# Kernel tuning notes

Measured on AMD Instinct MI355X. Metric: run time of the kernel, lower is better.

## Reference

```python
import jax, jax.numpy as jnp
import numpy as np
from jax import lax

B, S, E, DF, H, L, V, T = 32, 512, 512, 2048, 8, 2, 30000, 12
START, STOP = 10, 11
NEG = -10000.0


def setup_inputs() -> dict:
    key = jax.random.key(0)
    ks = jax.random.split(key, 12)
    g = lambda i, shape, sc=0.02: jax.random.normal(ks[i], shape, jnp.float32) * sc
    trans = jax.random.normal(ks[9], (T, T), jnp.float32)
    trans = trans.at[START, :].set(NEG).at[:, STOP].set(NEG)
    return {
        "sentence": jax.random.randint(ks[0], (B, S), 0, V),
        "seq_len": jax.random.randint(ks[1], (B,), 1, S + 1),
        "tags": jax.random.randint(ks[2], (B, S), 0, 10),
        "emb": g(3, (V, E), 1.0),
        "attn_in_w": g(4, (L, 3 * E, E)), "attn_in_b": jnp.zeros((L, 3 * E)),
        "attn_out_w": g(5, (L, E, E)), "attn_out_b": jnp.zeros((L, E)),
        "ln1_g": jnp.ones((L, E)), "ln1_b": jnp.zeros((L, E)),
        "ln2_g": jnp.ones((L, E)), "ln2_b": jnp.zeros((L, E)),
        "ff1_w": g(6, (L, DF, E)), "ff1_b": jnp.zeros((L, DF)),
        "ff2_w": g(7, (L, E, DF)), "ff2_b": jnp.zeros((L, E)),
        "tag_w": g(8, (T, E)), "tag_b": jnp.zeros((T,)),
        "transitions": trans,
    }


def _ln(x, g, b):
    m = x.mean(-1, keepdims=True)
    v = ((x - m) ** 2).mean(-1, keepdims=True)
    return (x - m) / jnp.sqrt(v + 1e-5) * g + b


def _mha(x, w_in, b_in, w_out, b_out):
    b_, s_, e_ = x.shape
    d = e_ // H
    qkv = x @ w_in.T + b_in
    q, k, v = jnp.split(qkv, 3, axis=-1)
    split = lambda t: t.reshape(b_, s_, H, d).transpose(0, 2, 1, 3)
    q, k, v = split(q), split(k), split(v)
    att = jax.nn.softmax(jnp.einsum('bhqd,bhkd->bhqk', q, k) / np.sqrt(d).astype(np.float32), axis=-1)
    o = jnp.einsum('bhqk,bhkd->bhqd', att, v).transpose(0, 2, 1, 3).reshape(b_, s_, e_)
    return o @ w_out.T + b_out


def _forward_impl(sentence, seq_len, tags, emb, attn_in_w, attn_in_b, attn_out_w,
                  attn_out_b, ln1_g, ln1_b, ln2_g, ln2_b, ff1_w, ff1_b, ff2_w,
                  ff2_b, tag_w, tag_b, transitions):
    # Transformer encoder features (dropout in eval mode -> identity)
    x = emb[sentence]  # (B,S,E)
    for l in range(L):
        x = _ln(x + _mha(x, attn_in_w[l], attn_in_b[l], attn_out_w[l], attn_out_b[l]), ln1_g[l], ln1_b[l])
        h = jax.nn.relu(x @ ff1_w[l].T + ff1_b[l]) @ ff2_w[l].T + ff2_b[l]
        x = _ln(x + h, ln2_g[l], ln2_b[l])
    feats = x @ tag_w.T + tag_b  # (B,S,T)

    # CRF forward algorithm (log-semiring scan, masked by seq_len)
    alpha0 = jnp.full((B, T), NEG, feats.dtype).at[:, START].set(0.0)

    def step(alpha, xs):
        emit_t, t = xs  # emit_t: (B,T)
        new = emit_t + jax.nn.logsumexp(alpha[:, None, :] + transitions[None, :, :], axis=-1)
        return jnp.where((t < seq_len)[:, None], new, alpha), None

    alpha, _ = lax.scan(step, alpha0, (feats.transpose(1, 0, 2), jnp.arange(S)))
    fwd_score = jax.nn.logsumexp(alpha + transitions[STOP][None, :], axis=-1)  # (B,)

    # gold score (vectorized _score_sentence)
    tags_ext = jnp.concatenate([jnp.full((B, 1), START, tags.dtype), tags], axis=1)  # (B,S+1)
    mask = jnp.arange(S)[None, :] < seq_len[:, None]  # (B,S)
    trans_sc = jnp.where(mask, transitions[tags_ext[:, 1:], tags_ext[:, :-1]], 0.0).sum(-1)
    emit_sc = jnp.where(mask, jnp.take_along_axis(feats, tags[:, :, None], axis=2)[..., 0], 0.0).sum(-1)
    last_tag = jnp.take_along_axis(tags_ext, seq_len[:, None], axis=1)[:, 0]
    gold = trans_sc + emit_sc + transitions[STOP, last_tag]

    return jnp.mean(fwd_score - gold)


def reference(sentence, seq_len, tags, emb, attn_in_w, attn_in_b, attn_out_w,
              attn_out_b, ln1_g, ln1_b, ln2_g, ln2_b, ff1_w, ff1_b, ff2_w,
              ff2_b, tag_w, tag_b, transitions):
    return _forward_impl(sentence, seq_len, tags, emb, attn_in_w, attn_in_b,
                         attn_out_w, attn_out_b, ln1_g, ln1_b, ln2_g, ln2_b,
                         ff1_w, ff1_b, ff2_w, ff2_b, tag_w, tag_b, transitions)
```

## Files before the change

### kernel.cpp

```cpp
#include <hip/hip_runtime.h>
#include <hip/hip_bf16.h>

#define BB 32
#define SSZ 512
#define EE 512
#define DFF 2048
#define HH 8
#define LL 2
#define TT 12
#define START_TAG 10
#define STOP_TAG 11
#define CB 8
#define CM (CB * SSZ)
#define NCHUNK (BB / CB)
#define NBH (CB * HH)
#define NBH_ALL (BB * HH)
#define NCHK 8

typedef __hip_bfloat16 bf16;
typedef __attribute__((ext_vector_type(8))) short short8;
typedef __attribute__((ext_vector_type(4))) float f32x4;

__device__ __forceinline__ float b2f(bf16 x) { return __bfloat162float(x); }
__device__ __forceinline__ float ldw(const void* p, size_t i, bool isbf) {
  return isbf ? __bfloat162float(((const bf16*)p)[i]) : ((const float*)p)[i];
}

__device__ __forceinline__ void gl_lds16(const bf16* g, bf16* l) {
  __builtin_amdgcn_global_load_lds(
      (const __attribute__((address_space(1))) void*)g,
      (__attribute__((address_space(3))) void*)l, 16, 0, 0);
}

__global__ void k_detect(const void* trans, int* dflag) {
  if (threadIdx.x == 0) {
    const unsigned short* u = (const unsigned short*)trans;
    dflag[0] = (u[START_TAG * TT] == 0xC61C && u[START_TAG * TT + 1] == 0xC61C) ? 1 : 0;
  }
}

__global__ void k_cvt(const void* src, bf16* dst, long n, const int* dflag) {
  bool isbf = dflag[0] != 0;
  for (long i = (long)blockIdx.x * 256 + threadIdx.x; i < n; i += (long)gridDim.x * 256)
    dst[i] = __float2bfloat16(ldw(src, i, isbf));
}

__global__ void k_embed(const int* sent, const void* emb, bf16* xb, const int* dflag) {
  bool isbf = dflag[0] != 0;
  int tok = blockIdx.x;
  int v = sent[tok];
  bf16* xo = xb + (size_t)tok * EE;
  for (int i = threadIdx.x; i < EE; i += 256)
    xo[i] = __float2bfloat16(ldw(emb, (size_t)v * EE + i, isbf));
}

__global__ __launch_bounds__(256) void k_mgemm(
    const bf16* __restrict__ A, const bf16* __restrict__ W,
    const void* __restrict__ bias, size_t boff, bf16* __restrict__ Cb,
    int M, int N, int K, int relu, const int* dflag) {
  bool isbf = dflag[0] != 0;
  __shared__ __align__(16) bf16 Sh[2 * 128 * 64];
  bf16* As = Sh;
  bf16* Bs = Sh + 128 * 64;
  const int tid = threadIdx.x;
  const int lane = tid & 63;
  const int wave = tid >> 6;
  const int wm = wave >> 1, wn = wave & 1;
  const int m0 = blockIdx.x * 128, n0 = blockIdx.y * 128;
  const int lrow = lane & 15, lk = lane >> 4;
  const int rl = lane >> 3, sl = lane & 7;

  f32x4 acc[4][4];
#pragma unroll
  for (int i = 0; i < 4; ++i)
#pragma unroll
    for (int j = 0; j < 4; ++j) acc[i][j] = (f32x4){0.f, 0.f, 0.f, 0.f};

  for (int kt = 0; kt < K; kt += 64) {
#pragma unroll
    for (int i = 0; i < 4; ++i) {
      int r = wave * 32 + i * 8 + rl;
      int gs = sl ^ (r & 7);
      gl_lds16(A + (size_t)(m0 + r) * K + kt + gs * 8, As + wave * 2048 + i * 512);
      gl_lds16(W + (size_t)(n0 + r) * K + kt + gs * 8, Bs + wave * 2048 + i * 512);
    }
    __syncthreads();
#pragma unroll
    for (int kb = 0; kb < 64; kb += 32) {
      short8 af[4], bfr[4];
#pragma unroll
      for (int mf = 0; mf < 4; ++mf) {
        int r = wm * 64 + mf * 16 + lrow;
        int ps = ((kb >> 3) + lk) ^ (r & 7);
        af[mf] = *(const short8*)&As[r * 64 + ps * 8];
      }
#pragma unroll
      for (int nf = 0; nf < 4; ++nf) {
        int r = wn * 64 + nf * 16 + lrow;
        int ps = ((kb >> 3) + lk) ^ (r & 7);
        bfr[nf] = *(const short8*)&Bs[r * 64 + ps * 8];
      }
#pragma unroll
      for (int mf = 0; mf < 4; ++mf)
#pragma unroll
        for (int nf = 0; nf < 4; ++nf)
          acc[mf][nf] = __builtin_amdgcn_mfma_f32_16x16x32_bf16(
              af[mf], bfr[nf], acc[mf][nf], 0, 0, 0);
    }
    __syncthreads();
  }
#pragma unroll
  for (int nf = 0; nf < 4; ++nf) {
    int nl = wn * 64 + nf * 16 + lrow;
    float bia = ldw(bias, boff + n0 + nl, isbf);
#pragma unroll
    for (int mf = 0; mf < 4; ++mf) {
#pragma unroll
      for (int r = 0; r < 4; ++r) {
        int ml = wm * 64 + mf * 16 + lk * 4 + r;
        float v = acc[mf][nf][r] + bia;
        if (relu) v = fmaxf(v, 0.f);
        Sh[ml * 128 + nl] = __float2bfloat16(v);
      }
    }
  }
  __syncthreads();
#pragma unroll
  for (int p = 0; p < 8; ++p) {
    int row = p * 16 + (tid >> 4);
    int off = (tid & 15) * 8;
    *(uint4*)(Cb + (size_t)(m0 + row) * N + n0 + off) = *(const uint4*)&Sh[row * 128 + off];
  }
}

__global__ void k_vt(const bf16* __restrict__ qkvb, bf16* __restrict__ vt) {
  int bh = blockIdx.y;
  int bl = bh >> 3, h = bh & 7;
  int k0 = blockIdx.x * 64;
  __shared__ bf16 t[64][72];
  int tid = threadIdx.x;
  int r = tid >> 2, cg = (tid & 3) * 16;
  const bf16* src = qkvb + ((size_t)(bl * SSZ + k0 + r)) * 1536 + 1024 + h * 64 + cg;
  *(uint4*)&t[r][cg] = *(const uint4*)src;
  *(uint4*)&t[r][cg + 8] = *(const uint4*)(src + 8);
  __syncthreads();
  int d = tid >> 2, kg = (tid & 3) * 16;
  bf16 tmp[16];
#pragma unroll
  for (int j = 0; j < 16; ++j) tmp[j] = t[kg + j][d];
  bf16* dst = vt + ((size_t)bh * 64 + d) * 512 + k0 + kg;
  *(uint4*)dst = *(uint4*)&tmp[0];
  *(uint4*)(dst + 8) = *(uint4*)&tmp[8];
}

#define LDK 68
#define LDP 72
__global__ __launch_bounds__(256) void k_flash(const bf16* __restrict__ qkv,
                                               const bf16* __restrict__ vt,
                                               bf16* __restrict__ ctx) {
  const int bh = blockIdx.x;
  const int bl = bh >> 3, h = bh & 7;
  const int m0 = blockIdx.y * 128;
  const int tid = threadIdx.x;
  const int lane = tid & 63;
  const int w = tid >> 6;
  const int lrow = lane & 15, lk = lane >> 4;

  __shared__ bf16 Ks[64 * LDK];
  __shared__ bf16 Vs[64 * LDK];
  __shared__ bf16 Ps[4][32 * LDP];

  short8 qf[2][2];
  {
    const bf16* Qb = qkv + (size_t)(bl * SSZ + m0 + w * 32) * 1536 + h * 64;
#pragma unroll
    for (int mf = 0; mf < 2; ++mf)
#pragma unroll
      for (int kb = 0; kb < 2; ++kb)
        qf[mf][kb] = *(const short8*)(Qb + (size_t)(mf * 16 + lrow) * 1536 + kb * 32 + lk * 8);
  }

  f32x4 acc_o[2][4];
  float lsum[2][4];
#pragma unroll
  for (int mf = 0; mf < 2; ++mf) {
#pragma unroll
    for (int nf = 0; nf < 4; ++nf) acc_o[mf][nf] = (f32x4){0.f, 0.f, 0.f, 0.f};
#pragma unroll
    for (int r = 0; r < 4; ++r) lsum[mf][r] = 0.f;
  }

  for (int kt = 0; kt < 8; ++kt) {
#pragma unroll
    for (int i = 0; i < 2; ++i) {
      int cc = tid + i * 256;
      int row = cc >> 3, seg = cc & 7;
      *(uint4*)&Ks[row * LDK + seg * 8] = *(const uint4*)(
          qkv + (size_t)(bl * SSZ + kt * 64 + row) * 1536 + 512 + h * 64 + seg * 8);
      *(uint4*)&Vs[row * LDK + seg * 8] = *(const uint4*)(
          vt + ((size_t)bh * 64 + row) * SSZ + kt * 64 + seg * 8);
    }
    __syncthreads();
    f32x4 s[2][4];
#pragma unroll
    for (int mf = 0; mf < 2; ++mf)
#pragma unroll
      for (int nf = 0; nf < 4; ++nf) s[mf][nf] = (f32x4){0.f, 0.f, 0.f, 0.f};
#pragma unroll
    for (int kb = 0; kb < 2; ++kb) {
      short8 bk[4];
#pragma unroll
      for (int nf = 0; nf < 4; ++nf)
        bk[nf] = *(const short8*)&Ks[(nf * 16 + lrow) * LDK + kb * 32 + lk * 8];
#pragma unroll
      for (int mf = 0; mf < 2; ++mf)
#pragma unroll
        for (int nf = 0; nf < 4; ++nf)
          s[mf][nf] = __builtin_amdgcn_mfma_f32_16x16x32_bf16(qf[mf][kb], bk[nf],
                                                              s[mf][nf], 0, 0, 0);
    }
#pragma unroll
    for (int mf = 0; mf < 2; ++mf)
#pragma unroll
      for (int r = 0; r < 4; ++r) {
        float p0 = __expf(0.125f * s[mf][0][r]);
        float p1 = __expf(0.125f * s[mf][1][r]);
        float p2 = __expf(0.125f * s[mf][2][r]);
        float p3 = __expf(0.125f * s[mf][3][r]);
        s[mf][0][r] = p0; s[mf][1][r] = p1; s[mf][2][r] = p2; s[mf][3][r] = p3;
        lsum[mf][r] += (p0 + p1) + (p2 + p3);
      }
#pragma unroll
    for (int mf = 0; mf < 2; ++mf)
#pragma unroll
      for (int nf = 0; nf < 4; ++nf)
#pragma unroll
        for (int r = 0; r < 4; ++r)
          Ps[w][(mf * 16 + lk * 4 + r) * LDP + nf * 16 + lrow] =
              __float2bfloat16(s[mf][nf][r]);
#pragma unroll
    for (int kb = 0; kb < 2; ++kb) {
      short8 ap[2], bv[4];
#pragma unroll
      for (int mf = 0; mf < 2; ++mf)
        ap[mf] = *(const short8*)&Ps[w][(mf * 16 + lrow) * LDP + kb * 32 + lk * 8];
#pragma unroll
      for (int nf = 0; nf < 4; ++nf)
        bv[nf] = *(const short8*)&Vs[(nf * 16 + lrow) * LDK + kb * 32 + lk * 8];
#pragma unroll
      for (int mf = 0; mf < 2; ++mf)
#pragma unroll
        for (int nf = 0; nf < 4; ++nf)
          acc_o[mf][nf] = __builtin_amdgcn_mfma_f32_16x16x32_bf16(ap[mf], bv[nf],
                                                                  acc_o[mf][nf], 0, 0, 0);
    }
    __syncthreads();
  }
#pragma unroll
  for (int mf = 0; mf < 2; ++mf) {
#pragma unroll
    for (int r = 0; r < 4; ++r) {
      float ls = lsum[mf][r];
      ls += __shfl_xor(ls, 1, 64);
      ls += __shfl_xor(ls, 2, 64);
      ls += __shfl_xor(ls, 4, 64);
      ls += __shfl_xor(ls, 8, 64);
      float inv = 1.f / ls;
      int q = m0 + w * 32 + mf * 16 + lk * 4 + r;
#pragma unroll
      for (int nf = 0; nf < 4; ++nf)
        ctx[((size_t)(bl * SSZ + q)) * EE + h * 64 + nf * 16 + lrow] =
            __float2bfloat16(acc_o[mf][nf][r] * inv);
    }
  }
}

__global__ void k_ln_res(bf16* xb, const bf16* hb, const void* g,
                         const void* be, size_t goff, const int* dflag) {
  bool isbf = dflag[0] != 0;
  int tok = blockIdx.x, tid = threadIdx.x;
  size_t base = (size_t)tok * EE;
  float v0 = b2f(xb[base + tid]) + b2f(hb[base + tid]);
  float v1 = b2f(xb[base + tid + 256]) + b2f(hb[base + tid + 256]);
  float s = v0 + v1, ss = v0 * v0 + v1 * v1;
#pragma unroll
  for (int off = 32; off > 0; off >>= 1) {
    s += __shfl_down(s, off, 64);
    ss += __shfl_down(ss, off, 64);
  }
  __shared__ float ps[4], pss[4];
  __shared__ float mean_s, rstd_s;
  int w = tid >> 6;
  if ((tid & 63) == 0) { ps[w] = s; pss[w] = ss; }
  __syncthreads();
  if (tid == 0) {
    float S_ = ps[0] + ps[1] + ps[2] + ps[3];
    float SS_ = pss[0] + pss[1] + pss[2] + pss[3];
    float mu = S_ / (float)EE;
    float var = SS_ / (float)EE - mu * mu;
    mean_s = mu;
    rstd_s = rsqrtf(var + 1e-5f);
  }
  __syncthreads();
  float mu = mean_s, rs = rstd_s;
  float r0 = (v0 - mu) * rs * ldw(g, goff + tid, isbf) + ldw(be, goff + tid, isbf);
  float r1 = (v1 - mu) * rs * ldw(g, goff + tid + 256, isbf) + ldw(be, goff + tid + 256, isbf);
  xb[base + tid] = __float2bfloat16(r0);
  xb[base + tid + 256] = __float2bfloat16(r1);
}

__global__ void k_feats(const bf16* xb, const bf16* tgw, const void* tgb,
                        float* feats, const int* dflag) {
  bool isbf = dflag[0] != 0;
  int m = blockIdx.x * 4 + (threadIdx.x >> 6);
  int lane = threadIdx.x & 63;
  uint4 raw = *(const uint4*)(xb + (size_t)m * EE + lane * 8);
  const bf16* rb = (const bf16*)&raw;
  float xv[8];
#pragma unroll
  for (int j = 0; j < 8; ++j) xv[j] = b2f(rb[j]);
#pragma unroll
  for (int t = 0; t < TT; ++t) {
    uint4 wraw = *(const uint4*)(tgw + t * EE + lane * 8);
    const bf16* wb = (const bf16*)&wraw;
    float s = 0.f;
#pragma unroll
    for (int j = 0; j < 8; ++j) s += xv[j] * b2f(wb[j]);
#pragma unroll
    for (int off = 32; off > 0; off >>= 1) s += __shfl_down(s, off, 64);
    if (lane == 0) feats[(size_t)m * TT + t] = s + ldw(tgb, t, isbf);
  }
}

__global__ void k_crf1(const float* feats, const int* seq_len, const void* trans_in,
                       float* cmat, const int* dflag) {
  bool isbf = dflag[0] != 0;
  int c = blockIdx.x, b = blockIdx.y;
  int tid = threadIdx.x;
  __shared__ float tr[144];
  __shared__ float abuf[2][144];
  if (tid < 144) tr[tid] = ldw(trans_in, tid, isbf);
  bool act = tid < 144;
  int i = tid / 12, j = tid % 12;
  if (act) abuf[0][tid] = (i == j) ? 0.f : -1e30f;
  __syncthreads();
  float trrow[12];
  if (act) {
#pragma unroll
    for (int k = 0; k < 12; ++k) trrow[k] = tr[i * 12 + k];
  }
  int len = seq_len[b];
  int t0 = c * 64;
  int t1 = min(len, t0 + 64);
  int cur = 0;
  for (int t = t0; t < t1; ++t) {
    float nv = 0.f;
    if (act) {
      float m = -1e30f, v[12];
#pragma unroll
      for (int k = 0; k < 12; ++k) {
        v[k] = trrow[k] + abuf[cur][k * 12 + j];
        m = fmaxf(m, v[k]);
      }
      float s = 0.f;
#pragma unroll
      for (int k = 0; k < 12; ++k) s += __expf(v[k] - m);
      nv = feats[((size_t)b * SSZ + t) * TT + i] + m + __logf(s);
    }
    if (act) abuf[cur ^ 1][tid] = nv;
    __syncthreads();
    cur ^= 1;
  }
  if (act) cmat[((size_t)b * NCHK + c) * 144 + tid] = abuf[cur][tid];
}

__global__ void k_crf2(const float* cmat, const float* feats, const int* tags,
                       const int* seq_len, const void* trans_in, float* bscore,
                       const int* dflag) {
  bool isbf = dflag[0] != 0;
  int b = blockIdx.x;
  int tid = threadIdx.x;
  __shared__ float tr[144];
  __shared__ float tbuf[2][144];
  __shared__ float alpha_sh[12];
  if (tid < 144) tr[tid] = ldw(trans_in, tid, isbf);
  bool act = tid < 144;
  int i = tid / 12, j = tid % 12;
  if (act) tbuf[0][tid] = cmat[((size_t)b * NCHK) * 144 + tid];
  __syncthreads();
  int cur = 0;
  for (int c = 1; c < NCHK; ++c) {
    float nv = 0.f;
    if (act) {
      const float* Cc = cmat + ((size_t)b * NCHK + c) * 144;
      float m = -1e30f, v[12];
#pragma unroll
      for (int k = 0; k < 12; ++k) {
        v[k] = Cc[i * 12 + k] + tbuf[cur][k * 12 + j];
        m = fmaxf(m, v[k]);
      }
      float s = 0.f;
#pragma unroll
      for (int k = 0; k < 12; ++k) s += __expf(v[k] - m);
      nv = m + __logf(s);
    }
    if (act) tbuf[cur ^ 1][tid] = nv;
    __syncthreads();
    cur ^= 1;
  }
  if (tid < 12) {
    float m = -1e30f, v[12];
#pragma unroll
    for (int k = 0; k < 12; ++k) {
      float a0 = (k == START_TAG) ? 0.f : -10000.f;
      v[k] = tbuf[cur][tid * 12 + k] + a0;
      m = fmaxf(m, v[k]);
    }
    float s = 0.f;
#pragma unroll
    for (int k = 0; k < 12; ++k) s += __expf(v[k] - m);
    alpha_sh[tid] = m + __logf(s);
  }
  __syncthreads();
  if (tid < 64) {
    int lane = tid;
    int len = seq_len[b];
    float part = 0.f;
    for (int s = lane; s < len; s += 64) {
      int ct = tags[b * SSZ + s];
      int pv = (s == 0) ? START_TAG : tags[b * SSZ + s - 1];
      part += tr[ct * 12 + pv] + feats[((size_t)b * SSZ + s) * TT + ct];
    }
#pragma unroll
    for (int off = 32; off > 0; off >>= 1) part += __shfl_down(part, off, 64);
    if (lane == 0) {
      float m = -1e30f;
#pragma unroll
      for (int k = 0; k < 12; ++k) m = fmaxf(m, alpha_sh[k] + tr[STOP_TAG * 12 + k]);
      float s = 0.f;
#pragma unroll
      for (int k = 0; k < 12; ++k) s += __expf(alpha_sh[k] + tr[STOP_TAG * 12 + k] - m);
      float fwd = m + __logf(s);
      int last = tags[b * SSZ + len - 1];
      bscore[b] = fwd - (part + tr[STOP_TAG * 12 + last]);
    }
  }
}

__global__ void k_final(const float* bscore, float* out) {
  int tid = threadIdx.x;
  float v = (tid < BB) ? bscore[tid] : 0.f;
#pragma unroll
  for (int off = 32; off > 0; off >>= 1) v += __shfl_down(v, off, 64);
  if (tid == 0) out[0] = v / (float)BB;
}

extern "C" void kernel_launch(void* const* d_in, const int* in_sizes, int n_in,
                              void* d_out, int out_size, void* d_ws, size_t ws_size,
                              hipStream_t stream) {
  const int* sentence = (const int*)d_in[0];
  const int* seq_len = (const int*)d_in[1];
  const int* tags = (const int*)d_in[2];
  const void* emb = d_in[3];
  const void* attn_in_w = d_in[4];
  const void* attn_in_b = d_in[5];
  const void* attn_out_w = d_in[6];
  const void* attn_out_b = d_in[7];
  const void* ln1_g = d_in[8];
  const void* ln1_b = d_in[9];
  const void* ln2_g = d_in[10];
  const void* ln2_b = d_in[11];
  const void* ff1_w = d_in[12];
  const void* ff1_b = d_in[13];
  const void* ff2_w = d_in[14];
  const void* ff2_b = d_in[15];
  const void* tag_w = d_in[16];
  const void* tag_b = d_in[17];
  const void* transitions = d_in[18];

  const int M = BB * SSZ;
  const size_t WEL = (size_t)LL * 3 * EE * EE + (size_t)LL * EE * EE +
                     (size_t)LL * DFF * EE + (size_t)LL * EE * DFF + (size_t)TT * EE;

  size_t o = 0;
  size_t f_feats = o; o += (size_t)M * TT;
  size_t f_bsc = o; o += 64;
  size_t f_cmat = o; o += (size_t)BB * NCHK * 144;
  size_t f_dflag = o; o += 16;
  size_t f_xb = o; o += (size_t)M * EE / 2;
  size_t f_hb = o; o += (size_t)M * EE / 2;
  size_t f_ctxb = o; o += (size_t)M * EE / 2;
  size_t f_act = o; o += (size_t)M * DFF / 2;
  size_t f_vt = o; o += (size_t)NBH_ALL * 64 * SSZ / 2;
  size_t f_w = o; o += (WEL + 1) / 2 + 8;
  size_t need_full = o * 4;
  bool full = ws_size >= need_full;

  float* ws = (float*)d_ws;
  if (full) {
    float* feats = ws + f_feats;
    float* bsc = ws + f_bsc;
    float* cmat = ws + f_cmat;
    int* dflag = (int*)(ws + f_dflag);
    bf16* xb = (bf16*)(ws + f_xb);
    bf16* hb = (bf16*)(ws + f_hb);
    bf16* ctxb = (bf16*)(ws + f_ctxb);
    bf16* act = (bf16*)(ws + f_act);
    bf16* vt = (bf16*)(ws + f_vt);
    bf16* w_aiw = (bf16*)(ws + f_w);
    bf16* w_aow = w_aiw + (size_t)LL * 3 * EE * EE;
    bf16* w_f1 = w_aow + (size_t)LL * EE * EE;
    bf16* w_f2 = w_f1 + (size_t)LL * DFF * EE;
    bf16* w_tg = w_f2 + (size_t)LL * EE * DFF;

    k_detect<<<dim3(1), dim3(64), 0, stream>>>(transitions, dflag);
    k_cvt<<<dim3(1024), dim3(256), 0, stream>>>(attn_in_w, w_aiw, (long)LL * 3 * EE * EE, dflag);
    k_cvt<<<dim3(512), dim3(256), 0, stream>>>(attn_out_w, w_aow, (long)LL * EE * EE, dflag);
    k_cvt<<<dim3(1024), dim3(256), 0, stream>>>(ff1_w, w_f1, (long)LL * DFF * EE, dflag);
    k_cvt<<<dim3(1024), dim3(256), 0, stream>>>(ff2_w, w_f2, (long)LL * EE * DFF, dflag);
    k_cvt<<<dim3(24), dim3(256), 0, stream>>>(tag_w, w_tg, (long)TT * EE, dflag);
    k_embed<<<dim3(M), dim3(256), 0, stream>>>(sentence, emb, xb, dflag);

    for (int l = 0; l < LL; ++l) {
      k_mgemm<<<dim3(M / 128, 12), dim3(256), 0, stream>>>(
          xb, w_aiw + (size_t)l * 3 * EE * EE, attn_in_b, (size_t)l * 3 * EE,
          act, M, 3 * EE, EE, 0, dflag);
      k_vt<<<dim3(8, NBH_ALL), dim3(256), 0, stream>>>(act, vt);
      k_flash<<<dim3(NBH_ALL, SSZ / 128), dim3(256), 0, stream>>>(act, vt, ctxb);
      k_mgemm<<<dim3(M / 128, 4), dim3(256), 0, stream>>>(
          ctxb, w_aow + (size_t)l * EE * EE, attn_out_b, (size_t)l * EE,
          hb, M, EE, EE, 0, dflag);
      k_ln_res<<<dim3(M), dim3(256), 0, stream>>>(xb, hb, ln1_g, ln1_b,
                                                  (size_t)l * EE, dflag);
      k_mgemm<<<dim3(M / 128, 16), dim3(256), 0, stream>>>(
          xb, w_f1 + (size_t)l * DFF * EE, ff1_b, (size_t)l * DFF,
          act, M, DFF, EE, 1, dflag);
      k_mgemm<<<dim3(M / 128, 4), dim3(256), 0, stream>>>(
          act, w_f2 + (size_t)l * EE * DFF, ff2_b, (size_t)l * EE,
          hb, M, EE, DFF, 0, dflag);
      k_ln_res<<<dim3(M), dim3(256), 0, stream>>>(xb, hb, ln2_g, ln2_b,
                                                  (size_t)l * EE, dflag);
    }
    k_feats<<<dim3(M / 4), dim3(256), 0, stream>>>(xb, w_tg, tag_b, feats, dflag);
    k_crf1<<<dim3(NCHK, BB), dim3(192), 0, stream>>>(feats, seq_len, transitions, cmat, dflag);
    k_crf2<<<dim3(BB), dim3(192), 0, stream>>>(cmat, feats, tags, seq_len, transitions, bsc, dflag);
    k_final<<<dim3(1), dim3(64), 0, stream>>>(bsc, (float*)d_out);
  } else {
    float* feats = ws;
    float* bsc = feats + (size_t)M * TT;
    float* cmat = bsc + 64;
    int* dflag = (int*)(cmat + (size_t)BB * NCHK * 144 + 16);
    bf16* xb = (bf16*)(dflag + 16);
    bf16* hb = xb + (size_t)M * EE;
    bf16* qkvb = hb + (size_t)CM * EE;
    bf16* ctxb = qkvb + (size_t)CM * 1536;
    bf16* ffh = ctxb + (size_t)CM * EE;
    bf16* vt = ffh + (size_t)CM * DFF;
    bf16* w_aiw = vt + (size_t)NBH * 64 * SSZ;
    bf16* w_aow = w_aiw + (size_t)LL * 3 * EE * EE;
    bf16* w_f1 = w_aow + (size_t)LL * EE * EE;
    bf16* w_f2 = w_f1 + (size_t)LL * DFF * EE;
    bf16* w_tg = w_f2 + (size_t)LL * EE * DFF;

    k_detect<<<dim3(1), dim3(64), 0, stream>>>(transitions, dflag);
    k_cvt<<<dim3(1024), dim3(256), 0, stream>>>(attn_in_w, w_aiw, (long)LL * 3 * EE * EE, dflag);
    k_cvt<<<dim3(512), dim3(256), 0, stream>>>(attn_out_w, w_aow, (long)LL * EE * EE, dflag);
    k_cvt<<<dim3(1024), dim3(256), 0, stream>>>(ff1_w, w_f1, (long)LL * DFF * EE, dflag);
    k_cvt<<<dim3(1024), dim3(256), 0, stream>>>(ff2_w, w_f2, (long)LL * EE * DFF, dflag);
    k_cvt<<<dim3(24), dim3(256), 0, stream>>>(tag_w, w_tg, (long)TT * EE, dflag);
    k_embed<<<dim3(M), dim3(256), 0, stream>>>(sentence, emb, xb, dflag);

    for (int l = 0; l < LL; ++l) {
      for (int c = 0; c < NCHUNK; ++c) {
        bf16* xbc = xb + (size_t)c * CM * EE;
        k_mgemm<<<dim3(CM / 128, 12), dim3(256), 0, stream>>>(
            xbc, w_aiw + (size_t)l * 3 * EE * EE, attn_in_b, (size_t)l * 3 * EE,
            qkvb, CM, 3 * EE, EE, 0, dflag);
        k_vt<<<dim3(8, NBH), dim3(256), 0, stream>>>(qkvb, vt);
        k_flash<<<dim3(NBH, SSZ / 128), dim3(256), 0, stream>>>(qkvb, vt, ctxb);
        k_mgemm<<<dim3(CM / 128, 4), dim3(256), 0, stream>>>(
            ctxb, w_aow + (size_t)l * EE * EE, attn_out_b, (size_t)l * EE,
            hb, CM, EE, EE, 0, dflag);
        k_ln_res<<<dim3(CM), dim3(256), 0, stream>>>(xbc, hb, ln1_g, ln1_b,
                                                     (size_t)l * EE, dflag);
        k_mgemm<<<dim3(CM / 128, 16), dim3(256), 0, stream>>>(
            xbc, w_f1 + (size_t)l * DFF * EE, ff1_b, (size_t)l * DFF,
            ffh, CM, DFF, EE, 1, dflag);
        k_mgemm<<<dim3(CM / 128, 4), dim3(256), 0, stream>>>(
            ffh, w_f2 + (size_t)l * EE * DFF, ff2_b, (size_t)l * EE,
            hb, CM, EE, DFF, 0, dflag);
        k_ln_res<<<dim3(CM), dim3(256), 0, stream>>>(xbc, hb, ln2_g, ln2_b,
                                                     (size_t)l * EE, dflag);
      }
    }
    k_feats<<<dim3(M / 4), dim3(256), 0, stream>>>(xb, w_tg, tag_b, feats, dflag);
    k_crf1<<<dim3(NCHK, BB), dim3(192), 0, stream>>>(feats, seq_len, transitions, cmat, dflag);
    k_crf2<<<dim3(BB), dim3(192), 0, stream>>>(cmat, feats, tags, seq_len, transitions, bsc, dflag);
    k_final<<<dim3(1), dim3(64), 0, stream>>>(bsc, (float*)d_out);
  }
}
```

Before: 728.0 us.

## Fuse V transpose into QKV GEMM epilogue and swizzle epilogue LDS

The QKV projection GEMM now writes its V-column tiles directly in transposed (per batch-head, d-major) layout into the vt buffer, so the separate k_vt transpose kernel and its launch are removed. The epilogue staging buffer also uses an XOR swizzle to reduce LDS bank conflicts on both the scatter and the vectorized readback. The cost is extra branching in the GEMM epilogue. V is still written to the qkv buffer only on non-V tiles; the V section of act is no longer filled, which is fine only if flash reads V solely from vt.

Measured after the change: 708.7 us. 1.03x faster.

```diff
diff --git a/kernel.cpp b/kernel.cpp
--- a/kernel.cpp
+++ b/kernel.cpp
@@ -32,6 +32,10 @@
       (__attribute__((address_space(3))) void*)l, 16, 0, 0);
 }
 
+__device__ __forceinline__ int swz(int row, int col) {
+  return row * 128 + (col ^ (((row >> 2) & 7) * 16));
+}
+
 __global__ void k_detect(const void* trans, int* dflag) {
   if (threadIdx.x == 0) {
     const unsigned short* u = (const unsigned short*)trans;
@@ -57,7 +61,7 @@
 __global__ __launch_bounds__(256) void k_mgemm(
     const bf16* __restrict__ A, const bf16* __restrict__ W,
     const void* __restrict__ bias, size_t boff, bf16* __restrict__ Cb,
-    int M, int N, int K, int relu, const int* dflag) {
+    bf16* __restrict__ vtout, int M, int N, int K, int relu, const int* dflag) {
   bool isbf = dflag[0] != 0;
   __shared__ __align__(16) bf16 Sh[2 * 128 * 64];
   bf16* As = Sh;
@@ -109,48 +113,59 @@
     }
     __syncthreads();
   }
-#pragma unroll
-  for (int nf = 0; nf < 4; ++nf) {
-    int nl = wn * 64 + nf * 16 + lrow;
-    float bia = ldw(bias, boff + n0 + nl, isbf);
-#pragma unroll
-    for (int mf = 0; mf < 4; ++mf) {
-#pragma unroll
-      for (int r = 0; r < 4; ++r) {
-        int ml = wm * 64 + mf * 16 + lk * 4 + r;
-        float v = acc[mf][nf][r] + bia;
-        if (relu) v = fmaxf(v, 0.f);
-        Sh[ml * 128 + nl] = __float2bfloat16(v);
-      }
-    }
-  }
-  __syncthreads();
-#pragma unroll
-  for (int p = 0; p < 8; ++p) {
-    int row = p * 16 + (tid >> 4);
-    int off = (tid & 15) * 8;
-    *(uint4*)(Cb + (size_t)(m0 + row) * N + n0 + off) = *(const uint4*)&Sh[row * 128 + off];
-  }
-}
-
-__global__ void k_vt(const bf16* __restrict__ qkvb, bf16* __restrict__ vt) {
-  int bh = blockIdx.y;
-  int bl = bh >> 3, h = bh & 7;
-  int k0 = blockIdx.x * 64;
-  __shared__ bf16 t[64][72];
-  int tid = threadIdx.x;
-  int r = tid >> 2, cg = (tid & 3) * 16;
-  const bf16* src = qkvb + ((size_t)(bl * SSZ + k0 + r)) * 1536 + 1024 + h * 64 + cg;
-  *(uint4*)&t[r][cg] = *(const uint4*)src;
-  *(uint4*)&t[r][cg + 8] = *(const uint4*)(src + 8);
-  __syncthreads();
-  int d = tid >> 2, kg = (tid & 3) * 16;
-  bf16 tmp[16];
-#pragma unroll
-  for (int j = 0; j < 16; ++j) tmp[j] = t[kg + j][d];
-  bf16* dst = vt + ((size_t)bh * 64 + d) * 512 + k0 + kg;
-  *(uint4*)dst = *(uint4*)&tmp[0];
-  *(uint4*)(dst + 8) = *(uint4*)&tmp[8];
+
+  const bool vpath = (vtout != nullptr) && (n0 >= 1024);
+  if (!vpath) {
+#pragma unroll
+    for (int nf = 0; nf < 4; ++nf) {
+      int nl = wn * 64 + nf * 16 + lrow;
+      float bia = ldw(bias, boff + n0 + nl, isbf);
+#pragma unroll
+      for (int mf = 0; mf < 4; ++mf) {
+#pragma unroll
+        for (int r = 0; r < 4; ++r) {
+          int ml = wm * 64 + mf * 16 + lk * 4 + r;
+          float v = acc[mf][nf][r] + bia;
+          if (relu) v = fmaxf(v, 0.f);
+          Sh[swz(ml, nl)] = __float2bfloat16(v);
+        }
+      }
+    }
+    __syncthreads();
+#pragma unroll
+    for (int p = 0; p < 8; ++p) {
+      int row = p * 16 + (tid >> 4);
+      int off = (tid & 15) * 8;
+      *(uint4*)(Cb + (size_t)(m0 + row) * N + n0 + off) =
+          *(const uint4*)&Sh[swz(row, off)];
+    }
+  } else {
+#pragma unroll
+    for (int nf = 0; nf < 4; ++nf) {
+      int nl = wn * 64 + nf * 16 + lrow;
+      float bia = ldw(bias, boff + n0 + nl, isbf);
+#pragma unroll
+      for (int mf = 0; mf < 4; ++mf) {
+        int mlb = wm * 64 + mf * 16 + lk * 4;
+        bf16 t4[4];
+#pragma unroll
+        for (int r = 0; r < 4; ++r) t4[r] = __float2bfloat16(acc[mf][nf][r] + bia);
+        *(uint2*)&Sh[swz(nl, mlb)] = *(const uint2*)t4;
+      }
+    }
+    __syncthreads();
+    int h0 = (n0 - 1024) >> 6;
+    int blb = (m0 >> 9) * 8;
+    int pos0 = m0 & 511;
+#pragma unroll
+    for (int p = 0; p < 8; ++p) {
+      int drow = p * 16 + (tid >> 4);
+      int poff = (tid & 15) * 8;
+      bf16* dst = vtout + ((size_t)(blb + h0 + (drow >> 6)) * 64 + (drow & 63)) * 512 +
+                  pos0 + poff;
+      *(uint4*)dst = *(const uint4*)&Sh[swz(drow, poff)];
+    }
+  }
 }
 
 #define LDK 68
@@ -524,20 +539,19 @@
     for (int l = 0; l < LL; ++l) {
       k_mgemm<<<dim3(M / 128, 12), dim3(256), 0, stream>>>(
           xb, w_aiw + (size_t)l * 3 * EE * EE, attn_in_b, (size_t)l * 3 * EE,
-          act, M, 3 * EE, EE, 0, dflag);
-      k_vt<<<dim3(8, NBH_ALL), dim3(256), 0, stream>>>(act, vt);
+          act, vt, M, 3 * EE, EE, 0, dflag);
       k_flash<<<dim3(NBH_ALL, SSZ / 128), dim3(256), 0, stream>>>(act, vt, ctxb);
       k_mgemm<<<dim3(M / 128, 4), dim3(256), 0, stream>>>(
           ctxb, w_aow + (size_t)l * EE * EE, attn_out_b, (size_t)l * EE,
-          hb, M, EE, EE, 0, dflag);
+          hb, (bf16*)nullptr, M, EE, EE, 0, dflag);
       k_ln_res<<<dim3(M), dim3(256), 0, stream>>>(xb, hb, ln1_g, ln1_b,
                                                   (size_t)l * EE, dflag);
       k_mgemm<<<dim3(M / 128, 16), dim3(256), 0, stream>>>(
           xb, w_f1 + (size_t)l * DFF * EE, ff1_b, (size_t)l * DFF,
-          act, M, DFF, EE, 1, dflag);
+          act, (bf16*)nullptr, M, DFF, EE, 1, dflag);
       k_mgemm<<<dim3(M / 128, 4), dim3(256), 0, stream>>>(
           act, w_f2 + (size_t)l * EE * DFF, ff2_b, (size_t)l * EE,
-          hb, M, EE, DFF, 0, dflag);
+          hb, (bf16*)nullptr, M, EE, DFF, 0, dflag);
       k_ln_res<<<dim3(M), dim3(256), 0, stream>>>(xb, hb, ln2_g, ln2_b,
                                                   (size_t)l * EE, dflag);
     }
@@ -575,20 +589,19 @@
         bf16* xbc = xb + (size_t)c * CM * EE;
         k_mgemm<<<dim3(CM / 128, 12), dim3(256), 0, stream>>>(
             xbc, w_aiw + (size_t)l * 3 * EE * EE, attn_in_b, (size_t)l * 3 * EE,
-            qkvb, CM, 3 * EE, EE, 0, dflag);
-        k_vt<<<dim3(8, NBH), dim3(256), 0, stream>>>(qkvb, vt);
+            qkvb, vt, CM, 3 * EE, EE, 0, dflag);
         k_flash<<<dim3(NBH, SSZ / 128), dim3(256), 0, stream>>>(qkvb, vt, ctxb);
         k_mgemm<<<dim3(CM / 128, 4), dim3(256), 0, stream>>>(
             ctxb, w_aow + (size_t)l * EE * EE, attn_out_b, (size_t)l * EE,
-            hb, CM, EE, EE, 0, dflag);
+            hb, (bf16*)nullptr, CM, EE, EE, 0, dflag);
         k_ln_res<<<dim3(CM), dim3(256), 0, stream>>>(xbc, hb, ln1_g, ln1_b,
                                                      (size_t)l * EE, dflag);
         k_mgemm<<<dim3(CM / 128, 16), dim3(256), 0, stream>>>(
             xbc, w_f1 + (size_t)l * DFF * EE, ff1_b, (size_t)l * DFF,
-            ffh, CM, DFF, EE, 1, dflag);
+            ffh, (bf16*)nullptr, CM, DFF, EE, 1, dflag);
         k_mgemm<<<dim3(CM / 128, 4), dim3(256), 0, stream>>>(
             ffh, w_f2 + (size_t)l * EE * DFF, ff2_b, (size_t)l * EE,
-            hb, CM, EE, DFF, 0, dflag);
+            hb, (bf16*)nullptr, CM, EE, DFF, 0, dflag);
         k_ln_res<<<dim3(CM), dim3(256), 0, stream>>>(xbc, hb, ln2_g, ln2_b,
                                                      (size_t)l * EE, dflag);
       }
```
